# Kernel tuning notes

Hardware: AMD Instinct MI355X
Metric: run time of the kernel (lower is better)

## Reference

```python
import jax, jax.numpy as jnp
import numpy as np

C = 256   # num_channels
H = 16    # num_heads
L = 16384 # protein length
W = 15    # window (odd -> same-length conv with pad=(W-1)//2)


def setup_inputs() -> dict:
    key = jax.random.key(0)
    k = jax.random.split(key, 5)
    x = jax.random.normal(k[0], (1, C, L), dtype=jnp.float32)
    w_heads = jax.random.normal(k[1], (H, C, W), dtype=jnp.float32) * (1.0 / np.sqrt(C * W))
    b_heads = jax.random.normal(k[2], (H,), dtype=jnp.float32) * 0.01
    # grouped 1x1 conv with groups=H: per-head [C_out, C_in] matrices
    w_tr = jax.random.normal(k[3], (H, C, C), dtype=jnp.float32) * (1.0 / np.sqrt(C))
    b_tr = jax.random.normal(k[4], (H, C), dtype=jnp.float32) * 0.01
    return {"x": x, "w_heads": w_heads, "b_heads": b_heads, "w_tr": w_tr, "b_tr": b_tr}


def reference(x, w_heads, b_heads, w_tr, b_tr):
    pad = (W - 1) // 2
    # conv_heads: Conv1d(C -> H, kernel W, pad (W-1)//2)  -> scores [1, H, L]
    scores = jax.lax.conv_general_dilated(
        x, w_heads, window_strides=(1,), padding=[(pad, pad)],
        dimension_numbers=("NCH", "OIH", "NCH"),
    ) + b_heads[None, :, None]
    # batchwise softmax over sequence (single protein in batch -> softmax over L)
    focuses = jax.nn.softmax(scores, axis=-1)  # [1, H, L]
    # outer product: [1, H, 1, L] * [1, 1, C, L] -> [1, H, C, L] (the big intermediate)
    focused = focuses[:, :, None, :] * x[:, None, :, :]
    # grouped 1x1 conv (per-head CxC matmul) then sum over heads -> [1, C, L]
    out = jnp.einsum("hoc,bhcl->bol", w_tr, focused)
    out = out + jnp.sum(b_tr, axis=0)[None, :, None]  # head-summed per-group bias
    return out
```

## Files before the change

### kernel.cpp

```cpp
#include <hip/hip_runtime.h>
#include <hip/hip_bf16.h>

#define L_LEN 16384
#define C_CH  256
#define H_HEADS 16
#define W_WIN 15

typedef __attribute__((ext_vector_type(8))) short bf16x8;
typedef __attribute__((ext_vector_type(4))) float f32x4;
typedef unsigned short ushort_t;


__device__ __forceinline__ void gll16(const void* g, void* l) {
    __builtin_amdgcn_global_load_lds(
        (const __attribute__((address_space(1))) void*)g,
        (__attribute__((address_space(3))) void*)l, 16, 0, 0);
}

__device__ __forceinline__ ushort_t f2bf(float f) {
    __hip_bfloat16 b = __float2bfloat16(f);
    return *(ushort_t*)&b;
}

__global__ __launch_bounds__(256) void k_transpose(const float* __restrict__ x,
                                                   ushort_t* __restrict__ xb) {
    __shared__ float tile[64][65];
    int t = threadIdx.x;
    int l0 = blockIdx.x * 64;
    int c0 = blockIdx.y * 64;
#pragma unroll
    for (int r = 0; r < 16; ++r) {
        int c = r * 4 + (t >> 6);
        int l = t & 63;
        tile[c][l] = x[(size_t)(c0 + c) * L_LEN + l0 + l];
    }
    __syncthreads();
    int l = t >> 2;
    int cq = (t & 3) * 16;
    ushort_t tmp[16];
#pragma unroll
    for (int i = 0; i < 16; ++i) tmp[i] = f2bf(tile[cq + i][l]);
    char* rowp = (char*)(xb + (size_t)(l0 + l) * C_CH);
    int swz = (l & 7) << 4;
    int b0 = (c0 + cq) * 2;
    *(uint4*)(rowp + (b0 ^ swz)) = *(uint4*)&tmp[0];
    *(uint4*)(rowp + ((b0 + 16) ^ swz)) = *(uint4*)&tmp[8];
}

__global__ __launch_bounds__(256) void k_aconv(const float* __restrict__ wtr,
                                               ushort_t* __restrict__ Ag) {
    int tid = blockIdx.x * 256 + threadIdx.x;
    size_t D = (size_t)tid * 16;
    int m = (int)(D >> 13);
    int inner = (int)(D & 8191);
    int kt = inner >> 7, wb = inner & 127;
    int ob = kt * 128 + (wb ^ ((m & 7) << 4));
    int k0 = ob >> 1;
    int h = k0 >> 8, c = k0 & 255;
    const float* src = wtr + ((size_t)h * C_CH + m) * C_CH + c;
    ushort_t tmp[8];
#pragma unroll
    for (int i = 0; i < 8; ++i) tmp[i] = f2bf(src[i]);
    *(uint4*)((char*)Ag + D) = *(uint4*)tmp;
}

__global__ __launch_bounds__(256) void k_wprep(const float* __restrict__ wh,
                                               ushort_t* __restrict__ awf) {
    int tid = blockIdx.x * 256 + threadIdx.x;
    int e = tid & 7;
    int lane = (tid >> 3) & 63;
    int ktw = tid >> 9;
    int w = ktw >> 3, kt = ktw & 7;
    int h = lane & 15;
    int c = kt * 32 + (lane >> 4) * 8 + e;
    awf[tid] = f2bf(wh[((size_t)h * C_CH + c) * W_WIN + w]);
}

__global__ __launch_bounds__(128) void k_convm(const ushort_t* __restrict__ xb,
                                               const ushort_t* __restrict__ awf,
                                               float* __restrict__ scores) {
    __shared__ char xs[48 * 512];
    int t = threadIdx.x;
    int n0 = blockIdx.x * 32;
#pragma unroll
    for (int i = 0; i < 12; ++i) {
        int chunk = t + i * 128;
        int rr = chunk >> 5;
        int cb = (chunk & 31) * 16;
        int l = n0 - 8 + rr;
        int lc = l < 0 ? 0 : (l >= L_LEN ? L_LEN - 1 : l);
        gll16((const char*)xb + (size_t)lc * 512 + cb, xs + chunk * 16);
    }
    __syncthreads();
    if (n0 == 0 || n0 == L_LEN - 32) {
        int rbase = (n0 == 0) ? 0 : 40;
        uint4 z = {0u, 0u, 0u, 0u};
#pragma unroll
        for (int i = 0; i < 2; ++i) {
            int ch = t + i * 128;
            *(uint4*)(xs + rbase * 512 + ch * 16) = z;
        }
        __syncthreads();
    }
    int wv = t >> 6, lane = t & 63;
    int r = lane & 15, q = lane >> 4;
    const f32x4 vzero = {0.f, 0.f, 0.f, 0.f};
    f32x4 acc[4] = {vzero, vzero, vzero, vzero};
    for (int w = 0; w < 15; ++w) {
        int rr = wv * 16 + r + w + 1;
        const char* rowp = &xs[rr * 512];
        int sw = (rr & 7) << 4;
#pragma unroll
        for (int kt = 0; kt < 8; ++kt) {
            bf16x8 a = *(const bf16x8*)(awf + (size_t)(((w * 8 + kt) * 64 + lane) * 8));
            bf16x8 b = *(const bf16x8*)(rowp + ((kt * 64 + q * 16) ^ sw));
            acc[kt & 3] = __builtin_amdgcn_mfma_f32_16x16x32_bf16(a, b, acc[kt & 3], 0, 0, 0);
        }
    }
    f32x4 s = acc[0] + acc[1] + acc[2] + acc[3];
    int nb = n0 + wv * 16;
#pragma unroll
    for (int e = 0; e < 4; ++e)
        scores[(size_t)(q * 4 + e) * L_LEN + nb + r] = s[e];
}

__global__ __launch_bounds__(1024) void k_stats(const float* __restrict__ scores,
                                                const float* __restrict__ btr,
                                                float2* __restrict__ MZ,
                                                float* __restrict__ bias) {
    int t = threadIdx.x;
    if (blockIdx.x == 16) {
        if (t < 256) {
            float s = 0.f;
#pragma unroll
            for (int h = 0; h < H_HEADS; ++h) s += btr[h * C_CH + t];
            bias[t] = s;
        }
        return;
    }
    __shared__ float red[17];
    int h = blockIdx.x;
    int wid = t >> 6, ln = t & 63;
    const float* sp = scores + (size_t)h * L_LEN;
    float v[16];
    float mx = -1e30f;
#pragma unroll
    for (int i = 0; i < 16; ++i) {
        v[i] = sp[i * 1024 + t];
        mx = fmaxf(mx, v[i]);
    }
    for (int o = 32; o > 0; o >>= 1) mx = fmaxf(mx, __shfl_xor(mx, o));
    if (ln == 0) red[wid] = mx;
    __syncthreads();
    if (t == 0) {
        float m2 = red[0];
        for (int i = 1; i < 16; ++i) m2 = fmaxf(m2, red[i]);
        red[16] = m2;
    }
    __syncthreads();
    float M = red[16];
    float s = 0.f;
#pragma unroll
    for (int i = 0; i < 16; ++i) s += __expf(v[i] - M);
    for (int o = 32; o > 0; o >>= 1) s += __shfl_xor(s, o);
    __syncthreads();
    if (ln == 0) red[wid] = s;
    __syncthreads();
    if (t == 0) {
        float Z = 0.f;
        for (int i = 0; i < 16; ++i) Z += red[i];
        float2 r; r.x = M; r.y = 1.0f / Z;
        MZ[h] = r;
    }
}

#define BRES 65536
#define ATS  16384
#define FTAB (BRES + 4 * ATS)

__global__ __launch_bounds__(256, 1) void k_gemm(const ushort_t* __restrict__ Ag,
                                                 const ushort_t* __restrict__ xb,
                                                 const float* __restrict__ scores,
                                                 const float2* __restrict__ MZ,
                                                 const float* __restrict__ bias,
                                                 float* __restrict__ out) {
    __shared__ char lds[FTAB + 8192];
    int t = threadIdx.x;
    int w = t >> 6, lane = t & 63;
    int m0 = blockIdx.y * 128, n0 = blockIdx.x * 128;
    int wr = w >> 1, wc = w & 1;
    int r = lane & 15, q = lane >> 4;

#pragma unroll
    for (int i = 0; i < 16; ++i) {
        int chunk = t + i * 256;
        int row = chunk >> 5, cb = (chunk & 31) * 16;
        gll16((const char*)xb + (size_t)(n0 + row) * 512 + cb, lds + chunk * 16);
    }
    {
        int idx = t * 8;
        int hh = idx >> 7, nn = idx & 127;
        float2 mz = MZ[hh];
        const float* sp = scores + (size_t)hh * L_LEN + n0 + nn;
        float* ft = (float*)(lds + FTAB);
#pragma unroll
        for (int e = 0; e < 8; ++e)
            ft[idx + e] = __expf(sp[e] - mz.x) * mz.y;
    }
    const f32x4 vzero = {0.f, 0.f, 0.f, 0.f};
    f32x4 oacc[4][4], hacc[4][4];
#pragma unroll
    for (int i = 0; i < 4; ++i)
#pragma unroll
        for (int j = 0; j < 4; ++j) { oacc[i][j] = vzero; hacc[i][j] = vzero; }

    __syncthreads();

    auto stageA = [&](int buf, int kt) {
        const char* src = (const char*)Ag + (size_t)(m0 + (t >> 3)) * 8192 + kt * 128 + (t & 7) * 16;
        char* dst = lds + BRES + buf * ATS + t * 16;
#pragma unroll
        for (int j = 0; j < 4; ++j)
            gll16(src + (size_t)j * 32 * 8192, dst + j * 4096);
    };
    auto compute = [&](int buf) {
        char* Ab = lds + BRES + buf * ATS;
        __builtin_amdgcn_s_setprio(1);
#pragma unroll
        for (int kk = 0; kk < 2; ++kk) {
            bf16x8 a[4], bb[4];
#pragma unroll
            for (int i = 0; i < 4; ++i) {
                int ar = wr * 64 + i * 16 + r;
                a[i] = *(const bf16x8*)(Ab + ar * 128 + ((kk * 64 + q * 16) ^ ((ar & 7) << 4)));
            }
#pragma unroll
            for (int j = 0; j < 4; ++j) {
                int br = wc * 64 + j * 16 + r;
                bb[j] = *(const bf16x8*)(lds + br * 512 +
                          ((buf * 0 + kk * 64 + q * 16)));
            }
            (void)bb;
#pragma unroll
            for (int i = 0; i < 4; ++i)
#pragma unroll
                for (int j = 0; j < 4; ++j)
                    hacc[i][j] = __builtin_amdgcn_mfma_f32_16x16x32_bf16(a[i], bb[j], hacc[i][j], 0, 0, 0);
        }
        __builtin_amdgcn_s_setprio(0);
    };
    (void)compute;

#define COMPUTE(BUF, QQ)                                                          \
    {                                                                             \
        char* Ab = lds + BRES + (BUF) * ATS;                                      \
        __builtin_amdgcn_s_setprio(1);                                            \
        _Pragma("unroll")                                                         \
        for (int kk = 0; kk < 2; ++kk) {                                          \
            bf16x8 a[4], bb[4];                                                   \
            _Pragma("unroll")                                                     \
            for (int i = 0; i < 4; ++i) {                                         \
                int ar = wr * 64 + i * 16 + r;                                    \
                a[i] = *(const bf16x8*)(Ab + ar * 128 +                           \
                          ((kk * 64 + q * 16) ^ ((ar & 7) << 4)));                \
            }                                                                     \
            _Pragma("unroll")                                                     \
            for (int j = 0; j < 4; ++j) {                                         \
                int br = wc * 64 + j * 16 + r;                                    \
                bb[j] = *(const bf16x8*)(lds + br * 512 +                         \
                          (((QQ) * 128 + kk * 64 + q * 16) ^ ((br & 7) << 4)));   \
            }                                                                     \
            _Pragma("unroll")                                                     \
            for (int i = 0; i < 4; ++i)                                           \
                _Pragma("unroll")                                                 \
                for (int j = 0; j < 4; ++j)                                       \
                    hacc[i][j] = __builtin_amdgcn_mfma_f32_16x16x32_bf16(         \
                        a[i], bb[j], hacc[i][j], 0, 0, 0);                        \
        }                                                                         \
        __builtin_amdgcn_s_setprio(0);                                            \
    }

#define SCALE(H)                                                                  \
    {                                                                             \
        const float* ft = (const float*)(lds + FTAB) + (H) * 128;                 \
        float f[4];                                                               \
        _Pragma("unroll")                                                         \
        for (int j = 0; j < 4; ++j) f[j] = ft[wc * 64 + j * 16 + r];              \
        _Pragma("unroll")                                                         \
        for (int i = 0; i < 4; ++i)                                               \
            _Pragma("unroll")                                                     \
            for (int j = 0; j < 4; ++j) {                                         \
                oacc[i][j] += hacc[i][j] * f[j];                                  \
                hacc[i][j] = vzero;                                               \
            }                                                                     \
    }

    stageA(0, 0); stageA(1, 1); stageA(2, 2);

    for (int h = 0; h < 15; ++h) {
#pragma unroll
        for (int qq = 0; qq < 4; ++qq) {
            int kt = h * 4 + qq;
            asm volatile("s_waitcnt vmcnt(8)" ::: "memory");
            __builtin_amdgcn_s_barrier();
            stageA((kt + 3) & 3, kt + 3);
            COMPUTE(kt & 3, qq);
        }
        SCALE(h);
    }
    asm volatile("s_waitcnt vmcnt(8)" ::: "memory");
    __builtin_amdgcn_s_barrier();
    stageA(3, 63);
    COMPUTE(0, 0);
    asm volatile("s_waitcnt vmcnt(8)" ::: "memory");
    __builtin_amdgcn_s_barrier();
    COMPUTE(1, 1);
    asm volatile("s_waitcnt vmcnt(4)" ::: "memory");
    __builtin_amdgcn_s_barrier();
    COMPUTE(2, 2);
    asm volatile("s_waitcnt vmcnt(0)" ::: "memory");
    __builtin_amdgcn_s_barrier();
    COMPUTE(3, 3);
    SCALE(15);

#pragma unroll
    for (int i = 0; i < 4; ++i) {
        int mrow = m0 + wr * 64 + i * 16 + q * 4;
        float4 bv = *(const float4*)&bias[mrow];
        float bvr[4] = {bv.x, bv.y, bv.z, bv.w};
#pragma unroll
        for (int j = 0; j < 4; ++j) {
            int n = n0 + wc * 64 + j * 16 + r;
#pragma unroll
            for (int rr = 0; rr < 4; ++rr)
                out[(size_t)(mrow + rr) * L_LEN + n] = oacc[i][j][rr] + bvr[rr];
        }
    }
#undef COMPUTE
#undef SCALE
}

extern "C" void kernel_launch(void* const* d_in, const int* in_sizes, int n_in,
                              void* d_out, int out_size, void* d_ws, size_t ws_size,
                              hipStream_t stream) {
    const float* x   = (const float*)d_in[0];
    const float* wh  = (const float*)d_in[1];
    const float* wtr = (const float*)d_in[3];
    const float* btr = (const float*)d_in[4];
    float* out = (float*)d_out;
    char* ws = (char*)d_ws;

    ushort_t* Ag     = (ushort_t*)(ws);
    ushort_t* xb     = (ushort_t*)(ws + ((size_t)2 << 20));
    float*    scores = (float*)(ws + ((size_t)10 << 20));
    ushort_t* awf    = (ushort_t*)(ws + ((size_t)11 << 20));
    char*     sc     = ws + ((size_t)11 << 20) + (128 << 10);
    float2*   MZ     = (float2*)(sc);
    float*    bias   = (float*)(sc + 1024);

    k_transpose<<<dim3(256, 4), 256, 0, stream>>>(x, xb);
    k_aconv<<<dim3(512), 256, 0, stream>>>(wtr, Ag);
    k_wprep<<<dim3(240), 256, 0, stream>>>(wh, awf);
    k_convm<<<dim3(512), 128, 0, stream>>>(xb, awf, scores);
    k_stats<<<dim3(17), 1024, 0, stream>>>(scores, btr, MZ, bias);
    k_gemm<<<dim3(128, 2), 256, 0, stream>>>(Ag, xb, scores, MZ, bias, out);
}
```

Baseline: 130.7 us.

## Merge prep kernels into one launch and use 8 waves per GEMM block

Three preprocessing kernels (x transpose, W_tr conversion, conv weight prep) are folded into one kernel that dispatches on block index, removing two launches. The GEMM block goes from 4 to 8 waves, each wave covering 64x32 of the output instead of 64x64. The A-tile staging, wait counts, B-tile loads and softmax-table fill are reshaped to match. This aims to hide latency better with more waves on only 256 blocks, at the cost of more redundant A-fragment LDS reads per MFMA.

```diff
diff --git a/kernel.cpp b/kernel.cpp
--- a/kernel.cpp
+++ b/kernel.cpp
@@ -22,58 +22,59 @@
     return *(ushort_t*)&b;
 }
 
-__global__ __launch_bounds__(256) void k_transpose(const float* __restrict__ x,
-                                                   ushort_t* __restrict__ xb) {
-    __shared__ float tile[64][65];
+__global__ __launch_bounds__(256) void k_prep(const float* __restrict__ x,
+                                              const float* __restrict__ wtr,
+                                              const float* __restrict__ wh,
+                                              ushort_t* __restrict__ xb,
+                                              ushort_t* __restrict__ Ag,
+                                              ushort_t* __restrict__ awf) {
+    int bid = blockIdx.x;
     int t = threadIdx.x;
-    int l0 = blockIdx.x * 64;
-    int c0 = blockIdx.y * 64;
-#pragma unroll
-    for (int r = 0; r < 16; ++r) {
-        int c = r * 4 + (t >> 6);
-        int l = t & 63;
-        tile[c][l] = x[(size_t)(c0 + c) * L_LEN + l0 + l];
-    }
-    __syncthreads();
-    int l = t >> 2;
-    int cq = (t & 3) * 16;
-    ushort_t tmp[16];
-#pragma unroll
-    for (int i = 0; i < 16; ++i) tmp[i] = f2bf(tile[cq + i][l]);
-    char* rowp = (char*)(xb + (size_t)(l0 + l) * C_CH);
-    int swz = (l & 7) << 4;
-    int b0 = (c0 + cq) * 2;
-    *(uint4*)(rowp + (b0 ^ swz)) = *(uint4*)&tmp[0];
-    *(uint4*)(rowp + ((b0 + 16) ^ swz)) = *(uint4*)&tmp[8];
-}
-
-__global__ __launch_bounds__(256) void k_aconv(const float* __restrict__ wtr,
-                                               ushort_t* __restrict__ Ag) {
-    int tid = blockIdx.x * 256 + threadIdx.x;
-    size_t D = (size_t)tid * 16;
-    int m = (int)(D >> 13);
-    int inner = (int)(D & 8191);
-    int kt = inner >> 7, wb = inner & 127;
-    int ob = kt * 128 + (wb ^ ((m & 7) << 4));
-    int k0 = ob >> 1;
-    int h = k0 >> 8, c = k0 & 255;
-    const float* src = wtr + ((size_t)h * C_CH + m) * C_CH + c;
-    ushort_t tmp[8];
-#pragma unroll
-    for (int i = 0; i < 8; ++i) tmp[i] = f2bf(src[i]);
-    *(uint4*)((char*)Ag + D) = *(uint4*)tmp;
-}
-
-__global__ __launch_bounds__(256) void k_wprep(const float* __restrict__ wh,
-                                               ushort_t* __restrict__ awf) {
-    int tid = blockIdx.x * 256 + threadIdx.x;
-    int e = tid & 7;
-    int lane = (tid >> 3) & 63;
-    int ktw = tid >> 9;
-    int w = ktw >> 3, kt = ktw & 7;
-    int h = lane & 15;
-    int c = kt * 32 + (lane >> 4) * 8 + e;
-    awf[tid] = f2bf(wh[((size_t)h * C_CH + c) * W_WIN + w]);
+    if (bid < 1024) {
+        __shared__ float tile[64][65];
+        int l0 = (bid & 255) * 64;
+        int c0 = (bid >> 8) * 64;
+#pragma unroll
+        for (int r = 0; r < 16; ++r) {
+            int c = r * 4 + (t >> 6);
+            int l = t & 63;
+            tile[c][l] = x[(size_t)(c0 + c) * L_LEN + l0 + l];
+        }
+        __syncthreads();
+        int l = t >> 2;
+        int cq = (t & 3) * 16;
+        ushort_t tmp[16];
+#pragma unroll
+        for (int i = 0; i < 16; ++i) tmp[i] = f2bf(tile[cq + i][l]);
+        char* rowp = (char*)(xb + (size_t)(l0 + l) * C_CH);
+        int swz = (l & 7) << 4;
+        int b0 = (c0 + cq) * 2;
+        *(uint4*)(rowp + (b0 ^ swz)) = *(uint4*)&tmp[0];
+        *(uint4*)(rowp + ((b0 + 16) ^ swz)) = *(uint4*)&tmp[8];
+    } else if (bid < 1536) {
+        int tid = (bid - 1024) * 256 + t;
+        size_t D = (size_t)tid * 16;
+        int m = (int)(D >> 13);
+        int inner = (int)(D & 8191);
+        int kt = inner >> 7, wb = inner & 127;
+        int ob = kt * 128 + (wb ^ ((m & 7) << 4));
+        int k0 = ob >> 1;
+        int h = k0 >> 8, c = k0 & 255;
+        const float* src = wtr + ((size_t)h * C_CH + m) * C_CH + c;
+        ushort_t tmp[8];
+#pragma unroll
+        for (int i = 0; i < 8; ++i) tmp[i] = f2bf(src[i]);
+        *(uint4*)((char*)Ag + D) = *(uint4*)tmp;
+    } else {
+        int tid = (bid - 1536) * 256 + t;
+        int e = tid & 7;
+        int lane = (tid >> 3) & 63;
+        int ktw = tid >> 9;
+        int w = ktw >> 3, kt = ktw & 7;
+        int h = lane & 15;
+        int c = kt * 32 + (lane >> 4) * 8 + e;
+        awf[tid] = f2bf(wh[((size_t)h * C_CH + c) * W_WIN + w]);
+    }
 }
 
 __global__ __launch_bounds__(128) void k_convm(const ushort_t* __restrict__ xb,
@@ -178,7 +179,7 @@
 #define ATS  16384
 #define FTAB (BRES + 4 * ATS)
 
-__global__ __launch_bounds__(256, 1) void k_gemm(const ushort_t* __restrict__ Ag,
+__global__ __launch_bounds__(512, 1) void k_gemm(const ushort_t* __restrict__ Ag,
                                                  const ushort_t* __restrict__ xb,
                                                  const float* __restrict__ scores,
                                                  const float2* __restrict__ MZ,
@@ -188,31 +189,31 @@
     int t = threadIdx.x;
     int w = t >> 6, lane = t & 63;
     int m0 = blockIdx.y * 128, n0 = blockIdx.x * 128;
-    int wr = w >> 1, wc = w & 1;
+    int wr = w >> 2, wc = w & 3;
     int r = lane & 15, q = lane >> 4;
 
 #pragma unroll
-    for (int i = 0; i < 16; ++i) {
-        int chunk = t + i * 256;
+    for (int i = 0; i < 8; ++i) {
+        int chunk = t + i * 512;
         int row = chunk >> 5, cb = (chunk & 31) * 16;
         gll16((const char*)xb + (size_t)(n0 + row) * 512 + cb, lds + chunk * 16);
     }
     {
-        int idx = t * 8;
+        int idx = t * 4;
         int hh = idx >> 7, nn = idx & 127;
         float2 mz = MZ[hh];
         const float* sp = scores + (size_t)hh * L_LEN + n0 + nn;
         float* ft = (float*)(lds + FTAB);
 #pragma unroll
-        for (int e = 0; e < 8; ++e)
+        for (int e = 0; e < 4; ++e)
             ft[idx + e] = __expf(sp[e] - mz.x) * mz.y;
     }
     const f32x4 vzero = {0.f, 0.f, 0.f, 0.f};
-    f32x4 oacc[4][4], hacc[4][4];
+    f32x4 oacc[4][2], hacc[4][2];
 #pragma unroll
     for (int i = 0; i < 4; ++i)
 #pragma unroll
-        for (int j = 0; j < 4; ++j) { oacc[i][j] = vzero; hacc[i][j] = vzero; }
+        for (int j = 0; j < 2; ++j) { oacc[i][j] = vzero; hacc[i][j] = vzero; }
 
     __syncthreads();
 
@@ -220,36 +221,9 @@
         const char* src = (const char*)Ag + (size_t)(m0 + (t >> 3)) * 8192 + kt * 128 + (t & 7) * 16;
         char* dst = lds + BRES + buf * ATS + t * 16;
 #pragma unroll
-        for (int j = 0; j < 4; ++j)
-            gll16(src + (size_t)j * 32 * 8192, dst + j * 4096);
+        for (int j = 0; j < 2; ++j)
+            gll16(src + (size_t)j * 64 * 8192, dst + j * 8192);
     };
-    auto compute = [&](int buf) {
-        char* Ab = lds + BRES + buf * ATS;
-        __builtin_amdgcn_s_setprio(1);
-#pragma unroll
-        for (int kk = 0; kk < 2; ++kk) {
-            bf16x8 a[4], bb[4];
-#pragma unroll
-            for (int i = 0; i < 4; ++i) {
-                int ar = wr * 64 + i * 16 + r;
-                a[i] = *(const bf16x8*)(Ab + ar * 128 + ((kk * 64 + q * 16) ^ ((ar & 7) << 4)));
-            }
-#pragma unroll
-            for (int j = 0; j < 4; ++j) {
-                int br = wc * 64 + j * 16 + r;
-                bb[j] = *(const bf16x8*)(lds + br * 512 +
-                          ((buf * 0 + kk * 64 + q * 16)));
-            }
-            (void)bb;
-#pragma unroll
-            for (int i = 0; i < 4; ++i)
-#pragma unroll
-                for (int j = 0; j < 4; ++j)
-                    hacc[i][j] = __builtin_amdgcn_mfma_f32_16x16x32_bf16(a[i], bb[j], hacc[i][j], 0, 0, 0);
-        }
-        __builtin_amdgcn_s_setprio(0);
-    };
-    (void)compute;
 
 #define COMPUTE(BUF, QQ)                                                          \
     {                                                                             \
@@ -257,7 +231,7 @@
         __builtin_amdgcn_s_setprio(1);                                            \
         _Pragma("unroll")                                                         \
         for (int kk = 0; kk < 2; ++kk) {                                          \
-            bf16x8 a[4], bb[4];                                                   \
+            bf16x8 a[4], bb[2];                                                   \
             _Pragma("unroll")                                                     \
             for (int i = 0; i < 4; ++i) {                                         \
                 int ar = wr * 64 + i * 16 + r;                                    \
@@ -265,15 +239,15 @@
                           ((kk * 64 + q * 16) ^ ((ar & 7) << 4)));                \
             }                                                                     \
             _Pragma("unroll")                                                     \
-            for (int j = 0; j < 4; ++j) {                                         \
-                int br = wc * 64 + j * 16 + r;                                    \
+            for (int j = 0; j < 2; ++j) {                                         \
+                int br = wc * 32 + j * 16 + r;                                    \
                 bb[j] = *(const bf16x8*)(lds + br * 512 +                         \
                           (((QQ) * 128 + kk * 64 + q * 16) ^ ((br & 7) << 4)));   \
             }                                                                     \
             _Pragma("unroll")                                                     \
             for (int i = 0; i < 4; ++i)                                           \
                 _Pragma("unroll")                                                 \
-                for (int j = 0; j < 4; ++j)                                       \
+                for (int j = 0; j < 2; ++j)                                       \
                     hacc[i][j] = __builtin_amdgcn_mfma_f32_16x16x32_bf16(         \
                         a[i], bb[j], hacc[i][j], 0, 0, 0);                        \
         }                                                                         \
@@ -283,13 +257,13 @@
 #define SCALE(H)                                                                  \
     {                                                                             \
         const float* ft = (const float*)(lds + FTAB) + (H) * 128;                 \
-        float f[4];                                                               \
+        float f[2];                                                               \
         _Pragma("unroll")                                                         \
-        for (int j = 0; j < 4; ++j) f[j] = ft[wc * 64 + j * 16 + r];              \
+        for (int j = 0; j < 2; ++j) f[j] = ft[wc * 32 + j * 16 + r];              \
         _Pragma("unroll")                                                         \
         for (int i = 0; i < 4; ++i)                                               \
             _Pragma("unroll")                                                     \
-            for (int j = 0; j < 4; ++j) {                                         \
+            for (int j = 0; j < 2; ++j) {                                         \
                 oacc[i][j] += hacc[i][j] * f[j];                                  \
                 hacc[i][j] = vzero;                                               \
             }                                                                     \
@@ -301,21 +275,21 @@
 #pragma unroll
         for (int qq = 0; qq < 4; ++qq) {
             int kt = h * 4 + qq;
-            asm volatile("s_waitcnt vmcnt(8)" ::: "memory");
+            asm volatile("s_waitcnt vmcnt(4)" ::: "memory");
             __builtin_amdgcn_s_barrier();
             stageA((kt + 3) & 3, kt + 3);
             COMPUTE(kt & 3, qq);
         }
         SCALE(h);
     }
-    asm volatile("s_waitcnt vmcnt(8)" ::: "memory");
+    asm volatile("s_waitcnt vmcnt(4)" ::: "memory");
     __builtin_amdgcn_s_barrier();
     stageA(3, 63);
     COMPUTE(0, 0);
-    asm volatile("s_waitcnt vmcnt(8)" ::: "memory");
+    asm volatile("s_waitcnt vmcnt(4)" ::: "memory");
     __builtin_amdgcn_s_barrier();
     COMPUTE(1, 1);
-    asm volatile("s_waitcnt vmcnt(4)" ::: "memory");
+    asm volatile("s_waitcnt vmcnt(2)" ::: "memory");
     __builtin_amdgcn_s_barrier();
     COMPUTE(2, 2);
     asm volatile("s_waitcnt vmcnt(0)" ::: "memory");
@@ -329,8 +303,8 @@
         float4 bv = *(const float4*)&bias[mrow];
         float bvr[4] = {bv.x, bv.y, bv.z, bv.w};
 #pragma unroll
-        for (int j = 0; j < 4; ++j) {
-            int n = n0 + wc * 64 + j * 16 + r;
+        for (int j = 0; j < 2; ++j) {
+            int n = n0 + wc * 32 + j * 16 + r;
 #pragma unroll
             for (int rr = 0; rr < 4; ++rr)
                 out[(size_t)(mrow + rr) * L_LEN + n] = oacc[i][j][rr] + bvr[rr];
@@ -358,10 +332,8 @@
     float2*   MZ     = (float2*)(sc);
     float*    bias   = (float*)(sc + 1024);
 
-    k_transpose<<<dim3(256, 4), 256, 0, stream>>>(x, xb);
-    k_aconv<<<dim3(512), 256, 0, stream>>>(wtr, Ag);
-    k_wprep<<<dim3(240), 256, 0, stream>>>(wh, awf);
+    k_prep<<<dim3(1776), 256, 0, stream>>>(x, wtr, wh, xb, Ag, awf);
     k_convm<<<dim3(512), 128, 0, stream>>>(xb, awf, scores);
     k_stats<<<dim3(17), 1024, 0, stream>>>(scores, btr, MZ, bias);
-    k_gemm<<<dim3(128, 2), 256, 0, stream>>>(Ag, xb, scores, MZ, bias, out);
-}
+    k_gemm<<<dim3(128, 2), 512, 0, stream>>>(Ag, xb, scores, MZ, bias, out);
+}
```

Result: faster. 122.9 us (-5.9%).
